# Performance work log

Measured on AMD Instinct MI355X. Metric: run time of the kernel, lower is better.

## Reference

```python
import jax, jax.numpy as jnp
import numpy as np

N_NODES = 100000

def setup_inputs() -> dict:
    key = jax.random.key(0)
    k1, k2, k3, k4, k5, k6 = jax.random.split(key, 6)
    input = jax.random.normal(k1, (N_NODES, 256), dtype=jnp.float32)
    weight = jax.random.normal(k2, (256, 256), dtype=jnp.float32) * (1.0 / np.sqrt(256))
    bias = jax.random.normal(k3, (256,), dtype=jnp.float32) * 0.02
    edge_rows = jax.random.randint(k4, (3200000,), 0, N_NODES, dtype=jnp.int32)
    edge_cols = jax.random.randint(k5, (3200000,), 0, N_NODES, dtype=jnp.int32)
    edge_vals = jax.random.uniform(k6, (3200000,), dtype=jnp.float32)
    return {"input": input, "weight": weight, "bias": bias,
            "edge_rows": edge_rows, "edge_cols": edge_cols, "edge_vals": edge_vals}

def reference(input, weight, bias, edge_rows, edge_cols, edge_vals):
    # support = X @ W  -- dense GEMM [N, in] x [in, out]
    support = input @ weight
    # output = spmm(adj, support): out[r] += adj[r,c] * support[c]
    gathered = support[edge_cols] * edge_vals[:, None]          # [E, out]
    output = jax.ops.segment_sum(gathered, edge_rows, num_segments=N_NODES)
    return output + bias
```

## Files before the change

kernel.cpp:

```cpp
#include <hip/hip_runtime.h>
#include <hip/hip_bf16.h>
#include <stdint.h>

#define M_NODES 100000
#define DIM     256
#define N_EDGES 3200000
#define CAP     80
#define CHUNK   4096
#define NCH     782
#define NB      391
#define BCAP    9216
#define NGB     1563

typedef __bf16 bf16x8 __attribute__((ext_vector_type(8)));
typedef float  f32x4  __attribute__((ext_vector_type(4)));
typedef unsigned short u16x8 __attribute__((ext_vector_type(8)));

__device__ __forceinline__ unsigned short f2bf(float f) {
    unsigned u = __float_as_uint(f);
    u += 0x7FFF + ((u >> 16) & 1);
    return (unsigned short)(u >> 16);
}

__global__ __launch_bounds__(256) void k_convert_wt(const float* __restrict__ W,
                                                    unsigned short* __restrict__ Wt,
                                                    int* __restrict__ cur) {
    int k = blockIdx.x, n = threadIdx.x;
    Wt[n * 256 + k] = f2bf(W[k * 256 + n]);
    int gid = k * 256 + n;
    for (int i = gid; i < NB * 32; i += 256 * 256) cur[i] = 0;
}

__global__ __launch_bounds__(256) void k_part2(const int* __restrict__ rows,
                                               const int* __restrict__ cols,
                                               const float* __restrict__ vals,
                                               uint64_t* __restrict__ part,
                                               int* __restrict__ cur) {
    __shared__ int cnt[NB];
    __shared__ int wcur[NB];
    int w = blockIdx.x, t = threadIdx.x;
    int base = w * CHUNK;
    int clen = N_EDGES - base; if (clen > CHUNK) clen = CHUNK;

    for (int i = t; i < NB; i += 256) cnt[i] = 0;
    __syncthreads();
    for (int i = t; i < clen; i += 256)
        atomicAdd(&cnt[rows[base + i] >> 8], 1);
    __syncthreads();

    for (int b = t; b < NB; b += 256)
        if (cnt[b]) wcur[b] = atomicAdd(&cur[b * 32], cnt[b]);
    __syncthreads();

    for (int i = t; i < clen; i += 256) {
        int   r = rows[base + i];
        int   c = cols[base + i];
        float v = vals[base + i];
        int   b = r >> 8;
        int pos = atomicAdd(&wcur[b], 1);
        if (pos < BCAP) {
            uint32_t lo = (uint32_t)c | ((uint32_t)(r & 255) << 17);
            part[(size_t)b * BCAP + pos] = ((uint64_t)__float_as_uint(v) << 32) | lo;
        }
    }
}

__global__ __launch_bounds__(1024) void k_build3(const uint64_t* __restrict__ part,
                                                 const int* __restrict__ cur,
                                                 uint32_t* __restrict__ csr4,
                                                 int* __restrict__ counts) {
    __shared__ int lcnt[256];
    int b = blockIdx.x, t = threadIdx.x;
    if (t < 256) lcnt[t] = 0;
    int n = cur[b * 32];
    if (n > BCAP) n = BCAP;
    __syncthreads();

    const uint64_t* p = part + (size_t)b * BCAP;
    for (int i = t; i < n; i += 1024) {
        uint64_t ent = p[i];
        uint32_t lo  = (uint32_t)ent;
        int   rl = (lo >> 17) & 255;
        int   c  = lo & 0x1FFFF;
        float v  = __uint_as_float((uint32_t)(ent >> 32));
        int qv = (int)(v * 32768.f + 0.5f);
        if (qv > 32767) qv = 32767;
        int pos = atomicAdd(&lcnt[rl], 1);
        if (pos < CAP)
            csr4[(size_t)(b * 256 + rl) * CAP + pos] = ((uint32_t)c << 15) | (uint32_t)qv;
    }
    __syncthreads();
    if (t < 256) counts[b * 256 + t] = lcnt[t];
}

__global__ __launch_bounds__(256) void k_gemm(const float* __restrict__ X,
                                              const unsigned short* __restrict__ Wt,
                                              signed char* __restrict__ Sq,
                                              float* __restrict__ scales) {
    int wave = threadIdx.x >> 6;
    int lane = threadIdx.x & 63;
    int tile = blockIdx.x * 4 + wave;
    if (tile >= M_NODES / 16) return;
    int m0   = tile * 16;
    int quad = lane >> 4;
    int r    = lane & 15;

    const float* aptr = X + (size_t)(m0 + r) * 256 + quad * 8;

    f32x4 acc[16];
#pragma unroll
    for (int t = 0; t < 16; ++t) acc[t] = {0.f, 0.f, 0.f, 0.f};

#pragma unroll
    for (int k0 = 0; k0 < 256; k0 += 32) {
        f32x4 a0 = *(const f32x4*)(aptr + k0);
        f32x4 a1 = *(const f32x4*)(aptr + k0 + 4);
        unsigned short au[8];
        au[0] = f2bf(a0.x); au[1] = f2bf(a0.y); au[2] = f2bf(a0.z); au[3] = f2bf(a0.w);
        au[4] = f2bf(a1.x); au[5] = f2bf(a1.y); au[6] = f2bf(a1.z); au[7] = f2bf(a1.w);
        bf16x8 a = *(bf16x8*)au;
#pragma unroll
        for (int t = 0; t < 16; ++t) {
            bf16x8 b = *(const bf16x8*)(Wt + (size_t)(t * 16 + r) * 256 + k0 + quad * 8);
            acc[t] = __builtin_amdgcn_mfma_f32_16x16x32_bf16(a, b, acc[t], 0, 0, 0);
        }
    }

    float pm[4] = {0.f, 0.f, 0.f, 0.f};
#pragma unroll
    for (int t = 0; t < 16; ++t)
#pragma unroll
        for (int i = 0; i < 4; ++i)
            pm[i] = fmaxf(pm[i], fabsf(acc[t][i]));
#pragma unroll
    for (int m = 1; m < 16; m <<= 1)
#pragma unroll
        for (int i = 0; i < 4; ++i)
            pm[i] = fmaxf(pm[i], __shfl_xor(pm[i], m));
    float inv[4];
#pragma unroll
    for (int i = 0; i < 4; ++i) {
        float mx = fmaxf(pm[i], 1e-20f);
        inv[i] = 127.f / mx;
        if (r == 0) scales[m0 + quad * 4 + i] = mx * (1.f / 127.f);
    }
#pragma unroll
    for (int t = 0; t < 16; ++t)
#pragma unroll
        for (int i = 0; i < 4; ++i) {
            int q = (int)rintf(acc[t][i] * inv[i]);
            Sq[(size_t)(m0 + quad * 4 + i) * 256 + t * 16 + r] = (signed char)q;
        }
}

__device__ __forceinline__ void accum_i8(float acc[8], uint2 s, float v) {
#pragma unroll
    for (int i = 0; i < 4; ++i)
        acc[i]     += (float)((signed char)(s.x >> (8 * i))) * v;
#pragma unroll
    for (int i = 0; i < 4; ++i)
        acc[4 + i] += (float)((signed char)(s.y >> (8 * i))) * v;
}

__global__ __launch_bounds__(256) void k_spmm(const int* __restrict__ counts,
                                              const uint32_t* __restrict__ csr4,
                                              const signed char* __restrict__ Sq,
                                              const float* __restrict__ scales,
                                              const float* __restrict__ bias,
                                              float* __restrict__ out) {
    int wave = threadIdx.x >> 6;
    int lane = threadIdx.x & 63;
    int r = blockIdx.x * 4 + wave;
    if (r >= M_NODES) return;
    int n = counts[r];
    if (n > CAP) n = CAP;
    const uint32_t* ep = csr4 + (size_t)r * CAP;
    int half = lane >> 5;
    int l    = lane & 31;

    float acc[8] = {0.f, 0.f, 0.f, 0.f, 0.f, 0.f, 0.f, 0.f};
    int j = 0;
    for (; j + 7 < n; j += 8) {
        uint32_t m0 = ep[j +     half];
        uint32_t m1 = ep[j + 2 + half];
        uint32_t m2 = ep[j + 4 + half];
        uint32_t m3 = ep[j + 6 + half];
        int c0 = m0 >> 15;  int c1 = m1 >> 15;
        int c2 = m2 >> 15;  int c3 = m3 >> 15;
        float v0 = (float)(m0 & 0x7FFF) * (1.f / 32768.f) * scales[c0];
        float v1 = (float)(m1 & 0x7FFF) * (1.f / 32768.f) * scales[c1];
        float v2 = (float)(m2 & 0x7FFF) * (1.f / 32768.f) * scales[c2];
        float v3 = (float)(m3 & 0x7FFF) * (1.f / 32768.f) * scales[c3];
        uint2 s0 = *(const uint2*)(Sq + (size_t)c0 * 256 + l * 8);
        uint2 s1 = *(const uint2*)(Sq + (size_t)c1 * 256 + l * 8);
        uint2 s2 = *(const uint2*)(Sq + (size_t)c2 * 256 + l * 8);
        uint2 s3 = *(const uint2*)(Sq + (size_t)c3 * 256 + l * 8);
        accum_i8(acc, s0, v0);
        accum_i8(acc, s1, v1);
        accum_i8(acc, s2, v2);
        accum_i8(acc, s3, v3);
    }
    for (; j + 1 < n; j += 2) {
        uint32_t m0 = ep[j + half];
        int c0 = m0 >> 15;
        float v0 = (float)(m0 & 0x7FFF) * (1.f / 32768.f) * scales[c0];
        uint2 s0 = *(const uint2*)(Sq + (size_t)c0 * 256 + l * 8);
        accum_i8(acc, s0, v0);
    }
    if (j < n && half == 0) {
        uint32_t m0 = ep[j];
        int c0 = m0 >> 15;
        float v0 = (float)(m0 & 0x7FFF) * (1.f / 32768.f) * scales[c0];
        uint2 s0 = *(const uint2*)(Sq + (size_t)c0 * 256 + l * 8);
        accum_i8(acc, s0, v0);
    }

#pragma unroll
    for (int i = 0; i < 8; ++i) acc[i] += __shfl(acc[i], lane + 32);

    if (half == 0) {
        f32x4 b0 = *(const f32x4*)(bias + l * 8);
        f32x4 b1 = *(const f32x4*)(bias + l * 8 + 4);
        f32x4 o0 = {acc[0] + b0.x, acc[1] + b0.y, acc[2] + b0.z, acc[3] + b0.w};
        f32x4 o1 = {acc[4] + b1.x, acc[5] + b1.y, acc[6] + b1.z, acc[7] + b1.w};
        float* op = out + (size_t)r * 256 + l * 8;
        __builtin_nontemporal_store(o0, (f32x4*)op);
        __builtin_nontemporal_store(o1, (f32x4*)(op + 4));
    }
}

extern "C" void kernel_launch(void* const* d_in, const int* in_sizes, int n_in,
                              void* d_out, int out_size, void* d_ws, size_t ws_size,
                              hipStream_t stream) {
    const float* X    = (const float*)d_in[0];
    const float* W    = (const float*)d_in[1];
    const float* bias = (const float*)d_in[2];
    const int*   er   = (const int*)d_in[3];
    const int*   ec   = (const int*)d_in[4];
    const float* ev   = (const float*)d_in[5];
    float* out = (float*)d_out;

    char* ws = (char*)d_ws;
    unsigned short* Wt     = (unsigned short*)ws;
    uint32_t*       csr4   = (uint32_t*)(ws + 131072);
    int*            cur    = (int*)(ws + 32161792);
    int*            counts = (int*)(ws + 32211840);
    float*          scales = (float*)(ws + 32612224);
    signed char*    Sq     = (signed char*)(ws + 33012608);
    uint64_t*       part   = (uint64_t*)(ws + 58637184);

    k_convert_wt<<<256,   256,  0, stream>>>(W, Wt, cur);
    k_part2     <<<NCH,   256,  0, stream>>>(er, ec, ev, part, cur);
    k_build3    <<<NB,    1024, 0, stream>>>(part, cur, csr4, counts);
    k_gemm      <<<NGB,   256,  0, stream>>>(X, Wt, Sq, scales);
    k_spmm      <<<25000, 256,  0, stream>>>(counts, csr4, Sq, scales, bias, out);
}
```

Before: 511.9 us.

## Stage bf16 weight in LDS and make GEMM blocks persistent over row tiles

The GEMM kernel now copies the whole 256x256 bf16 transposed weight (128 KB) into LDS once per block, using an XOR swizzle to avoid bank conflicts. It launches 256 blocks of 8 waves, and each block loops over 25 row tiles. Each wave prefetches its full X row slice into registers before the MFMA loop. This removes repeated global and L2 reads of the weight for every 16-row tile. The cost is a 128 KB LDS footprint that allows only one block per CU, plus higher register pressure from the prefetched operands.

```diff
diff --git a/kernel.cpp b/kernel.cpp
--- a/kernel.cpp
+++ b/kernel.cpp
@@ -10,7 +10,8 @@
 #define NCH     782
 #define NB      391
 #define BCAP    9216
-#define NGB     1563
+#define NGB     256
+#define NTILES  6250
 
 typedef __bf16 bf16x8 __attribute__((ext_vector_type(8)));
 typedef float  f32x4  __attribute__((ext_vector_type(4)));
@@ -93,64 +94,89 @@
     if (t < 256) counts[b * 256 + t] = lcnt[t];
 }
 
-__global__ __launch_bounds__(256) void k_gemm(const float* __restrict__ X,
+__global__ __launch_bounds__(512) void k_gemm(const float* __restrict__ X,
                                               const unsigned short* __restrict__ Wt,
                                               signed char* __restrict__ Sq,
                                               float* __restrict__ scales) {
-    int wave = threadIdx.x >> 6;
-    int lane = threadIdx.x & 63;
-    int tile = blockIdx.x * 4 + wave;
-    if (tile >= M_NODES / 16) return;
-    int m0   = tile * 16;
+    __shared__ unsigned short wlds[65536];
+    int t = threadIdx.x;
+
+#pragma unroll
+    for (int it = 0; it < 16; ++it) {
+        int f   = it * 512 + t;
+        int row = f >> 5;
+        int ci  = f & 31;
+        u16x8 v = *(const u16x8*)(Wt + row * 256 + ci * 8);
+        int lb  = (row * 512 + ci * 16) ^ ((row & 7) << 4);
+        *(u16x8*)((char*)wlds + lb) = v;
+    }
+    __syncthreads();
+
+    int w    = t >> 6;
+    int lane = t & 63;
     int quad = lane >> 4;
     int r    = lane & 15;
-
-    const float* aptr = X + (size_t)(m0 + r) * 256 + quad * 8;
-
-    f32x4 acc[16];
-#pragma unroll
-    for (int t = 0; t < 16; ++t) acc[t] = {0.f, 0.f, 0.f, 0.f};
-
-#pragma unroll
-    for (int k0 = 0; k0 < 256; k0 += 32) {
-        f32x4 a0 = *(const f32x4*)(aptr + k0);
-        f32x4 a1 = *(const f32x4*)(aptr + k0 + 4);
-        unsigned short au[8];
-        au[0] = f2bf(a0.x); au[1] = f2bf(a0.y); au[2] = f2bf(a0.z); au[3] = f2bf(a0.w);
-        au[4] = f2bf(a1.x); au[5] = f2bf(a1.y); au[6] = f2bf(a1.z); au[7] = f2bf(a1.w);
-        bf16x8 a = *(bf16x8*)au;
-#pragma unroll
-        for (int t = 0; t < 16; ++t) {
-            bf16x8 b = *(const bf16x8*)(Wt + (size_t)(t * 16 + r) * 256 + k0 + quad * 8);
-            acc[t] = __builtin_amdgcn_mfma_f32_16x16x32_bf16(a, b, acc[t], 0, 0, 0);
-        }
-    }
-
-    float pm[4] = {0.f, 0.f, 0.f, 0.f};
-#pragma unroll
-    for (int t = 0; t < 16; ++t)
-#pragma unroll
-        for (int i = 0; i < 4; ++i)
-            pm[i] = fmaxf(pm[i], fabsf(acc[t][i]));
-#pragma unroll
-    for (int m = 1; m < 16; m <<= 1)
-#pragma unroll
-        for (int i = 0; i < 4; ++i)
-            pm[i] = fmaxf(pm[i], __shfl_xor(pm[i], m));
-    float inv[4];
-#pragma unroll
-    for (int i = 0; i < 4; ++i) {
-        float mx = fmaxf(pm[i], 1e-20f);
-        inv[i] = 127.f / mx;
-        if (r == 0) scales[m0 + quad * 4 + i] = mx * (1.f / 127.f);
-    }
-#pragma unroll
-    for (int t = 0; t < 16; ++t)
+    int tile0 = blockIdx.x * 25;
+    int tend  = tile0 + 25; if (tend > NTILES) tend = NTILES;
+
+    for (int tile = tile0 + w; tile < tend; tile += 8) {
+        int m0 = tile * 16;
+        const float* ap = X + (size_t)(m0 + r) * 256 + quad * 8;
+
+        f32x4 xa[8], xb[8];
+#pragma unroll
+        for (int kk = 0; kk < 8; ++kk) {
+            xa[kk] = *(const f32x4*)(ap + kk * 32);
+            xb[kk] = *(const f32x4*)(ap + kk * 32 + 4);
+        }
+
+        f32x4 acc[16];
+#pragma unroll
+        for (int tt = 0; tt < 16; ++tt) acc[tt] = {0.f, 0.f, 0.f, 0.f};
+
+#pragma unroll
+        for (int kk = 0; kk < 8; ++kk) {
+            unsigned short au[8];
+            au[0] = f2bf(xa[kk].x); au[1] = f2bf(xa[kk].y);
+            au[2] = f2bf(xa[kk].z); au[3] = f2bf(xa[kk].w);
+            au[4] = f2bf(xb[kk].x); au[5] = f2bf(xb[kk].y);
+            au[6] = f2bf(xb[kk].z); au[7] = f2bf(xb[kk].w);
+            bf16x8 a = *(bf16x8*)au;
+#pragma unroll
+            for (int tt = 0; tt < 16; ++tt) {
+                int row = tt * 16 + r;
+                int lb  = (row * 512 + kk * 64 + quad * 16) ^ ((row & 7) << 4);
+                bf16x8 b = *(const bf16x8*)((char*)wlds + lb);
+                acc[tt] = __builtin_amdgcn_mfma_f32_16x16x32_bf16(a, b, acc[tt], 0, 0, 0);
+            }
+        }
+
+        float pm[4] = {0.f, 0.f, 0.f, 0.f};
+#pragma unroll
+        for (int tt = 0; tt < 16; ++tt)
+#pragma unroll
+            for (int i = 0; i < 4; ++i)
+                pm[i] = fmaxf(pm[i], fabsf(acc[tt][i]));
+#pragma unroll
+        for (int m = 1; m < 16; m <<= 1)
+#pragma unroll
+            for (int i = 0; i < 4; ++i)
+                pm[i] = fmaxf(pm[i], __shfl_xor(pm[i], m));
+        float inv[4];
 #pragma unroll
         for (int i = 0; i < 4; ++i) {
-            int q = (int)rintf(acc[t][i] * inv[i]);
-            Sq[(size_t)(m0 + quad * 4 + i) * 256 + t * 16 + r] = (signed char)q;
-        }
+            float mx = fmaxf(pm[i], 1e-20f);
+            inv[i] = 127.f / mx;
+            if (r == 0) scales[m0 + quad * 4 + i] = mx * (1.f / 127.f);
+        }
+#pragma unroll
+        for (int tt = 0; tt < 16; ++tt)
+#pragma unroll
+            for (int i = 0; i < 4; ++i) {
+                int q = (int)rintf(acc[tt][i] * inv[i]);
+                Sq[(size_t)(m0 + quad * 4 + i) * 256 + tt * 16 + r] = (signed char)q;
+            }
+    }
 }
 
 __device__ __forceinline__ void accum_i8(float acc[8], uint2 s, float v) {
@@ -252,6 +278,6 @@
     k_convert_wt<<<256,   256,  0, stream>>>(W, Wt, cur);
     k_part2     <<<NCH,   256,  0, stream>>>(er, ec, ev, part, cur);
     k_build3    <<<NB,    1024, 0, stream>>>(part, cur, csr4, counts);
-    k_gemm      <<<NGB,   256,  0, stream>>>(X, Wt, Sq, scales);
+    k_gemm      <<<NGB,   512,  0, stream>>>(X, Wt, Sq, scales);
     k_spmm      <<<25000, 256,  0, stream>>>(counts, csr4, Sq, scales, bias, out);
 }
```

Measured after the change: 638.0 us. 24.6% more time.
